# Kernel optimization log

Measured on AMD Instinct MI355X. Metric: run time of the kernel, lower is better.

## Reference

```python
import jax, jax.numpy as jnp
import numpy as np

N_NODES = 100000
N_EDGES = 1600000
F_IN = 128
HID = 128
N_CLASSES = 10
N_GRAPHS = 128
N_LAYERS = 4


def _uniform(key, shape, fan_in):
    s = 1.0 / np.sqrt(fan_in)
    return jax.random.uniform(key, shape, jnp.float32, -s, s)


def setup_inputs() -> dict:
    key = jax.random.key(0)
    ks = jax.random.split(key, 14)
    x = jax.random.normal(ks[0], (N_NODES, F_IN), jnp.float32)
    edge_index = jax.random.randint(ks[1], (2, N_EDGES), 0, N_NODES, dtype=jnp.int32)
    batch = jnp.sort(jax.random.randint(ks[2], (N_NODES,), 0, N_GRAPHS, dtype=jnp.int32))
    # GraphConv layer 1: lin_rel (with bias) + lin_root (no bias)
    W1_rel = _uniform(ks[3], (F_IN, HID), F_IN)
    b1_rel = _uniform(ks[4], (HID,), F_IN)
    W1_root = _uniform(ks[5], (F_IN, HID), F_IN)
    # remaining num_layers-1 GraphConv layers, stacked
    Wc_rel = _uniform(ks[6], (N_LAYERS - 1, HID, HID), HID)
    bc_rel = _uniform(ks[7], (N_LAYERS - 1, HID), HID)
    Wc_root = _uniform(ks[8], (N_LAYERS - 1, HID, HID), HID)
    # JumpingKnowledge 'cat' -> lin1: (num_layers*hidden) -> hidden
    Wl1 = _uniform(ks[9], (N_LAYERS * HID, HID), N_LAYERS * HID)
    bl1 = _uniform(ks[10], (HID,), N_LAYERS * HID)
    Wl2 = _uniform(ks[11], (HID, N_CLASSES), HID)
    bl2 = _uniform(ks[12], (N_CLASSES,), HID)
    return {
        "x": x, "edge_index": edge_index, "batch": batch,
        "W1_rel": W1_rel, "b1_rel": b1_rel, "W1_root": W1_root,
        "Wc_rel": Wc_rel, "bc_rel": bc_rel, "Wc_root": Wc_root,
        "Wl1": Wl1, "bl1": bl1, "Wl2": Wl2, "bl2": bl2,
    }


def reference(x, edge_index, batch, W1_rel, b1_rel, W1_root,
              Wc_rel, bc_rel, Wc_root, Wl1, bl1, Wl2, bl2):
    src, dst = edge_index[0], edge_index[1]

    def graph_conv(h, Wr, br, Wroot):
        # GraphConv (aggr='add'): lin_rel(sum_{j in N(i)} x_j) + lin_root(x_i)
        agg = jax.ops.segment_sum(h[src], dst, num_segments=N_NODES)
        return agg @ Wr + br + h @ Wroot

    counts = jax.ops.segment_sum(jnp.ones((N_NODES, 1), x.dtype), batch,
                                 num_segments=N_GRAPHS)
    counts = jnp.maximum(counts, 1.0)

    def global_mean_pool(h):
        sums = jax.ops.segment_sum(h, batch, num_segments=N_GRAPHS)
        return sums / counts

    h = jax.nn.relu(graph_conv(x, W1_rel, b1_rel, W1_root))
    xs = [global_mean_pool(h)]
    for i in range(N_LAYERS - 1):
        h = jax.nn.relu(graph_conv(h, Wc_rel[i], bc_rel[i], Wc_root[i]))
        xs.append(global_mean_pool(h))

    z = jnp.concatenate(xs, axis=-1)            # [N_GRAPHS, N_LAYERS*HID]
    z = jax.nn.relu(z @ Wl1 + bl1)
    return z @ Wl2 + bl2                        # [N_GRAPHS, N_CLASSES]
```

## Files before the change

kernel.cpp:

```cpp
#include <hip/hip_runtime.h>

#define NNODES 100000
#define NEDGES 1600000
#define FDIM 128
#define NGRAPHS 128
#define NLAYERS 4
#define NCLASS 10
#define LDC 136
#define LDC8 136
#define NBUCK 391
#define EBCAP 5120
#define EPB 4096
#define NBLK_E ((NEDGES + EPB - 1) / EPB)

typedef __attribute__((ext_vector_type(8))) short bf16x8;
typedef __attribute__((ext_vector_type(4))) float f32x4;
typedef __attribute__((ext_vector_type(2))) float f32x2;
typedef unsigned char u8;
typedef unsigned short u16;
typedef unsigned int u32;
typedef unsigned long long u64;

__device__ __forceinline__ u16 f2bf(float f) {
    u32 u = __float_as_uint(f);
    u += 0x7fffu + ((u >> 16) & 1u);
    return (u16)(u >> 16);
}
__device__ __forceinline__ u32 pack_bf(float a, float b) {
    return (u32)f2bf(a) | ((u32)f2bf(b) << 16);
}

__device__ __forceinline__ void gload_lds16(const u16* g, u16* l) {
    __builtin_amdgcn_global_load_lds(
        (const __attribute__((address_space(1))) u32*)g,
        (__attribute__((address_space(3))) u32*)l, 16, 0, 0);
}


__global__ __launch_bounds__(256) void conv_x(const float* __restrict__ x,
                                              u16* __restrict__ xb,
                                              u8* __restrict__ x8) {
    int i = (blockIdx.x * 256 + threadIdx.x) * 4;
    if (i < NNODES * FDIM) {
        float4 v = *(const float4*)(x + i);
        u32 p0 = pack_bf(v.x, v.y), p1 = pack_bf(v.z, v.w);
        *(u32*)(xb + i) = p0;
        *(u32*)(xb + i + 2) = p1;
        u32 a = (u32)__builtin_amdgcn_cvt_pk_fp8_f32(v.x, v.y, 0, 0);
        u32 b = (u32)__builtin_amdgcn_cvt_pk_fp8_f32(v.z, v.w, 0, 0);
        *(u32*)(x8 + i) = (a & 0xffffu) | (b << 16);
    }
}

__global__ __launch_bounds__(256) void conv_w(const float* __restrict__ W1_rel,
                                              const float* __restrict__ W1_root,
                                              const float* __restrict__ Wc_rel,
                                              const float* __restrict__ Wc_root,
                                              u16* __restrict__ Wcat) {
    int idx = blockIdx.x * 256 + threadIdx.x;
    if (idx >= NLAYERS * 256 * FDIM) return;
    int n = idx & 127;
    int k = (idx >> 7) & 255;
    int l = idx >> 15;
    const float* Wr = (l == 0) ? W1_rel  : Wc_rel  + (size_t)(l - 1) * FDIM * FDIM;
    const float* Wt = (l == 0) ? W1_root : Wc_root + (size_t)(l - 1) * FDIM * FDIM;
    float v = (k < 128) ? Wr[(size_t)k * FDIM + n] : Wt[(size_t)(k - 128) * FDIM + n];
    Wcat[(size_t)l * 32768 + (size_t)n * 256 + k] = f2bf(v);
}


__global__ __launch_bounds__(192) void graph_ptr_kernel(const int* __restrict__ batch,
                                                        int* __restrict__ gptr) {
    int g = threadIdx.x;
    if (g > NGRAPHS) return;
    int lo = 0, hi = NNODES;
    while (lo < hi) {
        int mid = (lo + hi) >> 1;
        if (batch[mid] < g) lo = mid + 1; else hi = mid;
    }
    gptr[g] = lo;
}

__global__ __launch_bounds__(256) void bcur_init(int* __restrict__ bcur) {
    int i = blockIdx.x * 256 + threadIdx.x;
    if (i < NBUCK) bcur[i] = i * EBCAP;
}

__global__ __launch_bounds__(256) void bucket_scatter(const int* __restrict__ src,
                                                      const int* __restrict__ dst,
                                                      int* __restrict__ bcur,
                                                      u64* __restrict__ ebuf) {
    __shared__ int cnt[NBUCK];
    for (int i = threadIdx.x; i < NBUCK; i += 256) cnt[i] = 0;
    __syncthreads();
    int e0 = blockIdx.x * EPB;
    int e1 = e0 + EPB; if (e1 > NEDGES) e1 = NEDGES;
    for (int e = e0 + threadIdx.x; e < e1; e += 256)
        atomicAdd(&cnt[dst[e] >> 8], 1);
    __syncthreads();
    for (int i = threadIdx.x; i < NBUCK; i += 256) {
        int c = cnt[i];
        if (c) cnt[i] = atomicAdd(&bcur[i], c);
    }
    __syncthreads();
    for (int e = e0 + threadIdx.x; e < e1; e += 256) {
        int d = dst[e], s = src[e];
        int pos = atomicAdd(&cnt[d >> 8], 1);
        ebuf[pos] = ((u64)(u32)d << 32) | (u32)s;
    }
}

__global__ __launch_bounds__(256) void bucket_csr(const u64* __restrict__ ebuf,
                                                  const int* __restrict__ bcur,
                                                  int* __restrict__ rowstart,
                                                  int* __restrict__ rowend,
                                                  int* __restrict__ csr) {
    __shared__ int cur[256];
    __shared__ int sd[256];
    int b = blockIdx.x, t = threadIdx.x;
    int ebase = b * EBCAP, eend = bcur[b];
    int n0 = b << 8;
    cur[t] = 0;
    __syncthreads();
    for (int e = ebase + t; e < eend; e += 256) {
        int d = (int)(ebuf[e] >> 32);
        atomicAdd(&cur[d & 255], 1);
    }
    __syncthreads();
    int v = cur[t];
    sd[t] = v;
    __syncthreads();
    for (int s = 1; s < 256; s <<= 1) {
        int add = (t >= s) ? sd[t - s] : 0;
        __syncthreads();
        sd[t] += add;
        __syncthreads();
    }
    int excl = sd[t] - v;
    cur[t] = ebase + excl;
    if (n0 + t < NNODES) {
        rowstart[n0 + t] = ebase + excl;
        rowend[n0 + t]   = ebase + excl + v;
    }
    __syncthreads();
    for (int e = ebase + t; e < eend; e += 256) {
        u64 r = ebuf[e];
        int d = (int)(r >> 32);
        int pos = atomicAdd(&cur[d & 255], 1);
        csr[pos] = (int)(r & 0xffffffffu);
    }
}


__global__ __launch_bounds__(256) void agg_bf(const u8* __restrict__ h8,
                                              const int* __restrict__ rowstart,
                                              const int* __restrict__ rowend,
                                              const int* __restrict__ csr,
                                              u16* __restrict__ agg) {
    int wave = threadIdx.x >> 6;
    int lane = threadIdx.x & 63;
    int node = (blockIdx.x << 2) + wave;
    if (node >= NNODES) return;
    int e0 = rowstart[node], e1 = rowend[node];
    int cnt = e1 - e0;
    float ax = 0.f, ay = 0.f;
    if (cnt <= 64) {
        int myidx = (lane < cnt) ? csr[e0 + lane] : 0;
        int nb = (cnt + 15) >> 4;
        for (int b = 0; b < nb; ++b) {
            int base = b * 16;
            u32 vv[16];
#pragma unroll
            for (int i = 0; i < 16; ++i) {
                int s = __builtin_amdgcn_readlane(myidx, base + i);
                vv[i] = *(const u16*)(h8 + (size_t)s * FDIM + lane * 2);
            }
            if (base + 16 <= cnt) {
#pragma unroll
                for (int i = 0; i < 16; ++i) {
                    f32x2 f = __builtin_amdgcn_cvt_pk_f32_fp8((int)vv[i], 0);
                    ax += f.x; ay += f.y;
                }
            } else {
#pragma unroll
                for (int i = 0; i < 16; ++i) {
                    f32x2 f = __builtin_amdgcn_cvt_pk_f32_fp8((int)vv[i], 0);
                    float m = (base + i < cnt) ? 1.f : 0.f;
                    ax = fmaf(f.x, m, ax);
                    ay = fmaf(f.y, m, ay);
                }
            }
        }
    } else {
        int e = e0;
        for (; e + 8 <= e1; e += 8) {
            u32 v0 = *(const u16*)(h8 + (size_t)csr[e]     * FDIM + lane * 2);
            u32 v1 = *(const u16*)(h8 + (size_t)csr[e + 1] * FDIM + lane * 2);
            u32 v2 = *(const u16*)(h8 + (size_t)csr[e + 2] * FDIM + lane * 2);
            u32 v3 = *(const u16*)(h8 + (size_t)csr[e + 3] * FDIM + lane * 2);
            u32 v4 = *(const u16*)(h8 + (size_t)csr[e + 4] * FDIM + lane * 2);
            u32 v5 = *(const u16*)(h8 + (size_t)csr[e + 5] * FDIM + lane * 2);
            u32 v6 = *(const u16*)(h8 + (size_t)csr[e + 6] * FDIM + lane * 2);
            u32 v7 = *(const u16*)(h8 + (size_t)csr[e + 7] * FDIM + lane * 2);
            f32x2 f0 = __builtin_amdgcn_cvt_pk_f32_fp8((int)v0, 0);
            f32x2 f1 = __builtin_amdgcn_cvt_pk_f32_fp8((int)v1, 0);
            f32x2 f2 = __builtin_amdgcn_cvt_pk_f32_fp8((int)v2, 0);
            f32x2 f3 = __builtin_amdgcn_cvt_pk_f32_fp8((int)v3, 0);
            f32x2 f4 = __builtin_amdgcn_cvt_pk_f32_fp8((int)v4, 0);
            f32x2 f5 = __builtin_amdgcn_cvt_pk_f32_fp8((int)v5, 0);
            f32x2 f6 = __builtin_amdgcn_cvt_pk_f32_fp8((int)v6, 0);
            f32x2 f7 = __builtin_amdgcn_cvt_pk_f32_fp8((int)v7, 0);
            ax += f0.x + f1.x + f2.x + f3.x + f4.x + f5.x + f6.x + f7.x;
            ay += f0.y + f1.y + f2.y + f3.y + f4.y + f5.y + f6.y + f7.y;
        }
        for (; e < e1; ++e) {
            u32 v0 = *(const u16*)(h8 + (size_t)csr[e] * FDIM + lane * 2);
            f32x2 f = __builtin_amdgcn_cvt_pk_f32_fp8((int)v0, 0);
            ax += f.x; ay += f.y;
        }
    }
    ((u32*)(agg + (size_t)node * FDIM))[lane] = pack_bf(ax, ay);
}


__global__ __launch_bounds__(256) void gemm_mfma(const u16* __restrict__ aggb,
                                                 const u16* __restrict__ hinb,
                                                 const u16* __restrict__ Wl,
                                                 const float* __restrict__ bias,
                                                 const int* __restrict__ batch,
                                                 float* __restrict__ z, int layer, int last,
                                                 u16* __restrict__ houtb,
                                                 u8* __restrict__ hout8) {
    __shared__ u16 S[26112];
    __shared__ int batchs[128];
    u16* As = S;
    u16* Bs = S + 8192;
    u8* Cs8 = (u8*)S + 34816;
    const int t = threadIdx.x;
    const int lane = t & 63;
    const int w = t >> 6;
    const int wr = w >> 1, wc = w & 1;
    const int row0 = blockIdx.x * 128;
    const int lr = lane & 15;

    const int srow = lane >> 3;
    const int sq = lane & 7;

    f32x4 acc[4][4];
#pragma unroll
    for (int m = 0; m < 4; ++m)
#pragma unroll
        for (int n = 0; n < 4; ++n) acc[m][n] = (f32x4){0.f, 0.f, 0.f, 0.f};

    if (t < 128) batchs[t] = (row0 + t < NNODES) ? batch[row0 + t] : NGRAPHS;

    for (int kb = 0; kb < 4; ++kb) {
        const u16* xsrc = (kb < 2) ? aggb : hinb;
        const int koff = (kb & 1) * 64;
#pragma unroll
        for (int i = 0; i < 4; ++i) {
            int blk8 = w * 4 + i;
            int r = blk8 * 8 + srow;
            int sc = sq ^ (r & 7);
            int arow = row0 + r; if (arow > NNODES - 1) arow = NNODES - 1;
            gload_lds16(xsrc + (size_t)arow * FDIM + koff + sc * 8, As + blk8 * 512);
            gload_lds16(Wl + (size_t)r * 256 + kb * 64 + sc * 8, Bs + blk8 * 512);
        }
        __syncthreads();
#pragma unroll
        for (int ks = 0; ks < 2; ++ks) {
            bf16x8 a[4], b[4];
            int qr = ks * 4 + (lane >> 4);
#pragma unroll
            for (int m = 0; m < 4; ++m) {
                int r = wr * 64 + m * 16 + lr;
                int ch = qr ^ (r & 7);
                a[m] = *(const bf16x8*)&As[r * 64 + ch * 8];
            }
#pragma unroll
            for (int n = 0; n < 4; ++n) {
                int r = wc * 64 + n * 16 + lr;
                int ch = qr ^ (r & 7);
                b[n] = *(const bf16x8*)&Bs[r * 64 + ch * 8];
            }
#pragma unroll
            for (int m = 0; m < 4; ++m)
#pragma unroll
                for (int n = 0; n < 4; ++n)
                    acc[m][n] = __builtin_amdgcn_mfma_f32_16x16x32_bf16(a[m], b[n], acc[m][n], 0, 0, 0);
        }
        __syncthreads();
    }
#pragma unroll
    for (int m = 0; m < 4; ++m) {
#pragma unroll
        for (int n = 0; n < 4; ++n) {
            int col = wc * 64 + n * 16 + lr;
            float bb = bias[col];
#pragma unroll
            for (int reg = 0; reg < 4; ++reg) {
                int row = wr * 64 + m * 16 + (lane >> 4) * 4 + reg;
                float v = fmaxf(acc[m][n][reg] + bb, 0.f);
                S[row * LDC + col] = f2bf(v);
                Cs8[row * LDC8 + col] = (u8)__builtin_amdgcn_cvt_pk_fp8_f32(v, v, 0, 0);
            }
        }
    }
    __syncthreads();
    if (!last) {
        int r = t >> 1, half = t & 1;
        if (row0 + r < NNODES) {
#pragma unroll
            for (int j = 0; j < 8; ++j) {
                bf16x8 v = *(const bf16x8*)&S[r * LDC + half * 64 + j * 8];
                *(bf16x8*)(houtb + (size_t)(row0 + r) * FDIM + half * 64 + j * 8) = v;
            }
#pragma unroll
            for (int j = 0; j < 8; ++j) {
                u64 v8 = *(const u64*)&Cs8[r * LDC8 + half * 64 + j * 8];
                *(u64*)(hout8 + (size_t)(row0 + r) * FDIM + half * 64 + j * 8) = v8;
            }
        }
    }
    {
        int col = t & 127, half = t >> 7;
        int r0 = half * 64, r1 = r0 + 64;
        float* zl = z + (size_t)layer * FDIM + col;
        int g = batchs[r0];
        float s = 0.f;
        for (int r = r0; r < r1; ++r) {
            int gn = batchs[r];
            if (gn != g) {
                atomicAdd(zl + (size_t)g * (NLAYERS * FDIM), s);
                s = 0.f; g = gn;
            }
            s += __uint_as_float((u32)S[r * LDC + col] << 16);
        }
        atomicAdd(zl + (size_t)g * (NLAYERS * FDIM), s);
    }
}


__global__ __launch_bounds__(128) void mlp1(const float* __restrict__ z,
                                            const int* __restrict__ gptr,
                                            const float* __restrict__ Wl1,
                                            const float* __restrict__ bl1,
                                            float* __restrict__ z2) {
    int g = blockIdx.x, j = threadIdx.x;
    __shared__ float zs[NLAYERS * FDIM];
    int cnt = gptr[g + 1] - gptr[g]; if (cnt < 1) cnt = 1;
    float invc = 1.0f / (float)cnt;
    for (int k = j; k < NLAYERS * FDIM; k += 128)
        zs[k] = z[(size_t)g * (NLAYERS * FDIM) + k] * invc;
    __syncthreads();
    float s = bl1[j];
    for (int k = 0; k < NLAYERS * FDIM; ++k) s = fmaf(zs[k], Wl1[(size_t)k * FDIM + j], s);
    z2[(size_t)g * FDIM + j] = fmaxf(s, 0.f);
}

__global__ __launch_bounds__(128) void mlp2(const float* __restrict__ z2,
                                            const float* __restrict__ Wl2,
                                            const float* __restrict__ bl2,
                                            float* __restrict__ out) {
    int g = blockIdx.x, c = threadIdx.x;
    __shared__ float zs[FDIM];
    if (threadIdx.x < FDIM) zs[threadIdx.x] = z2[(size_t)g * FDIM + threadIdx.x];
    __syncthreads();
    if (c < NCLASS) {
        float s = bl2[c];
        for (int k = 0; k < FDIM; ++k) s = fmaf(zs[k], Wl2[(size_t)k * NCLASS + c], s);
        out[(size_t)g * NCLASS + c] = s;
    }
}


extern "C" void kernel_launch(void* const* d_in, const int* in_sizes, int n_in,
                              void* d_out, int out_size, void* d_ws, size_t ws_size,
                              hipStream_t stream) {
    const float* x       = (const float*)d_in[0];
    const int*   ei      = (const int*)d_in[1];
    const int*   batch   = (const int*)d_in[2];
    const float* W1_rel  = (const float*)d_in[3];
    const float* b1_rel  = (const float*)d_in[4];
    const float* W1_root = (const float*)d_in[5];
    const float* Wc_rel  = (const float*)d_in[6];
    const float* bc_rel  = (const float*)d_in[7];
    const float* Wc_root = (const float*)d_in[8];
    const float* Wl1     = (const float*)d_in[9];
    const float* bl1     = (const float*)d_in[10];
    const float* Wl2     = (const float*)d_in[11];
    const float* bl2     = (const float*)d_in[12];
    float* out = (float*)d_out;

    const int* srcv = ei;
    const int* dstv = ei + NEDGES;

    char* ws = (char*)d_ws;
    size_t off = 0;
    auto alloc = [&](size_t bytes) -> void* {
        void* p = ws + off;
        off = (off + bytes + 255) & ~(size_t)255;
        return p;
    };
    u16* xb      = (u16*)alloc((size_t)NNODES * FDIM * 2);
    u16* hA      = (u16*)alloc((size_t)NNODES * FDIM * 2);
    u16* hB      = (u16*)alloc((size_t)NNODES * FDIM * 2);
    u16* aggb    = (u16*)alloc((size_t)NNODES * FDIM * 2);
    u8*  x8      = (u8*)alloc((size_t)NNODES * FDIM);
    u8*  h8A     = (u8*)alloc((size_t)NNODES * FDIM);
    u8*  h8B     = (u8*)alloc((size_t)NNODES * FDIM);
    u16* Wcat    = (u16*)alloc((size_t)NLAYERS * 256 * FDIM * 2);
    int* csr     = (int*)alloc((size_t)NBUCK * EBCAP * 4);
    int* rowstart= (int*)alloc((size_t)NNODES * 4);
    int* rowend  = (int*)alloc((size_t)NNODES * 4);
    int* bcur    = (int*)alloc((size_t)(NBUCK + 1) * 4);
    int* gptr    = (int*)alloc(1024);
    float* z     = (float*)alloc((size_t)(NGRAPHS + 1) * NLAYERS * FDIM * 4);
    float* z2    = (float*)alloc((size_t)NGRAPHS * FDIM * 4);
    u64* ebuf    = (u64*)hA;
    (void)ws_size; (void)in_sizes; (void)n_in; (void)out_size;

    hipMemsetAsync(z, 0, (size_t)(NGRAPHS + 1) * NLAYERS * FDIM * 4, stream);
    conv_x<<<(NNODES * FDIM / 4 + 255) / 256, 256, 0, stream>>>(x, xb, x8);
    conv_w<<<(NLAYERS * 256 * FDIM + 255) / 256, 256, 0, stream>>>(W1_rel, W1_root, Wc_rel, Wc_root, Wcat);
    graph_ptr_kernel<<<1, 192, 0, stream>>>(batch, gptr);
    bcur_init<<<(NBUCK + 255) / 256, 256, 0, stream>>>(bcur);
    bucket_scatter<<<NBLK_E, 256, 0, stream>>>(srcv, dstv, bcur, ebuf);
    bucket_csr<<<NBUCK, 256, 0, stream>>>(ebuf, bcur, rowstart, rowend, csr);

    const u16* hin = xb;
    const u8*  hin8 = x8;
    for (int l = 0; l < NLAYERS; ++l) {
        u16* hout  = (l & 1) ? hB : hA;
        u8*  hout8 = (l & 1) ? h8B : h8A;
        const u16* Wl = Wcat + (size_t)l * 256 * FDIM;
        const float* bb = (l == 0) ? b1_rel : bc_rel + (size_t)(l - 1) * FDIM;
        agg_bf<<<(NNODES + 3) / 4, 256, 0, stream>>>(hin8, rowstart, rowend, csr, aggb);
        gemm_mfma<<<(NNODES + 127) / 128, 256, 0, stream>>>(aggb, hin, Wl, bb, batch, z, l,
                                                            (l == NLAYERS - 1) ? 1 : 0, hout, hout8);
        hin = hout; hin8 = hout8;
    }
    mlp1<<<NGRAPHS, 128, 0, stream>>>(z, gptr, Wl1, bl1, z2);
    mlp2<<<NGRAPHS, 128, 0, stream>>>(z2, Wl2, bl2, out);
}
```

Measured before the change: 383.1 us.

## Halve GEMM epilogue LDS, stage bucket edges in LDS, merge setup kernels

The GEMM epilogue now stages output in two 64-row passes, which shrinks the shared buffer from about 52KB to 32KB so more blocks can be resident per CU. The cost is extra barriers and serialized epilogue phases. bucket_csr copies its bucket's edges into a 40KB LDS array so global ebuf is read once instead of twice, though that large LDS footprint limits its occupancy. The graph-pointer and bucket-cursor init kernels are merged into one launch.

New measurement: 410.9 us. +7.3%, slower.

```diff
diff --git a/kernel.cpp b/kernel.cpp
--- a/kernel.cpp
+++ b/kernel.cpp
@@ -69,21 +69,19 @@
 }
 
 
-__global__ __launch_bounds__(192) void graph_ptr_kernel(const int* __restrict__ batch,
-                                                        int* __restrict__ gptr) {
-    int g = threadIdx.x;
-    if (g > NGRAPHS) return;
-    int lo = 0, hi = NNODES;
-    while (lo < hi) {
-        int mid = (lo + hi) >> 1;
-        if (batch[mid] < g) lo = mid + 1; else hi = mid;
-    }
-    gptr[g] = lo;
-}
-
-__global__ __launch_bounds__(256) void bcur_init(int* __restrict__ bcur) {
-    int i = blockIdx.x * 256 + threadIdx.x;
-    if (i < NBUCK) bcur[i] = i * EBCAP;
+__global__ __launch_bounds__(512) void setup_kernel(const int* __restrict__ batch,
+                                                    int* __restrict__ gptr,
+                                                    int* __restrict__ bcur) {
+    int t = threadIdx.x;
+    if (t < NBUCK) bcur[t] = t * EBCAP;
+    if (t <= NGRAPHS) {
+        int lo = 0, hi = NNODES;
+        while (lo < hi) {
+            int mid = (lo + hi) >> 1;
+            if (batch[mid] < t) lo = mid + 1; else hi = mid;
+        }
+        gptr[t] = lo;
+    }
 }
 
 __global__ __launch_bounds__(256) void bucket_scatter(const int* __restrict__ src,
@@ -115,15 +113,18 @@
                                                   int* __restrict__ rowstart,
                                                   int* __restrict__ rowend,
                                                   int* __restrict__ csr) {
+    __shared__ u64 eb[EBCAP];
     __shared__ int cur[256];
     __shared__ int sd[256];
     int b = blockIdx.x, t = threadIdx.x;
     int ebase = b * EBCAP, eend = bcur[b];
+    int ne = eend - ebase;
     int n0 = b << 8;
     cur[t] = 0;
-    __syncthreads();
-    for (int e = ebase + t; e < eend; e += 256) {
-        int d = (int)(ebuf[e] >> 32);
+    for (int e = t; e < ne; e += 256) eb[e] = ebuf[ebase + e];
+    __syncthreads();
+    for (int e = t; e < ne; e += 256) {
+        int d = (int)(eb[e] >> 32);
         atomicAdd(&cur[d & 255], 1);
     }
     __syncthreads();
@@ -143,8 +144,8 @@
         rowend[n0 + t]   = ebase + excl + v;
     }
     __syncthreads();
-    for (int e = ebase + t; e < eend; e += 256) {
-        u64 r = ebuf[e];
+    for (int e = t; e < ne; e += 256) {
+        u64 r = eb[e];
         int d = (int)(r >> 32);
         int pos = atomicAdd(&cur[d & 255], 1);
         csr[pos] = (int)(r & 0xffffffffu);
@@ -231,11 +232,11 @@
                                                  float* __restrict__ z, int layer, int last,
                                                  u16* __restrict__ houtb,
                                                  u8* __restrict__ hout8) {
-    __shared__ u16 S[26112];
+    __shared__ u16 S[16384];
     __shared__ int batchs[128];
     u16* As = S;
     u16* Bs = S + 8192;
-    u8* Cs8 = (u8*)S + 34816;
+    u8* Cs8 = (u8*)S + 17408;
     const int t = threadIdx.x;
     const int lane = t & 63;
     const int w = t >> 6;
@@ -292,51 +293,57 @@
         __syncthreads();
     }
 #pragma unroll
-    for (int m = 0; m < 4; ++m) {
-#pragma unroll
-        for (int n = 0; n < 4; ++n) {
-            int col = wc * 64 + n * 16 + lr;
-            float bb = bias[col];
-#pragma unroll
-            for (int reg = 0; reg < 4; ++reg) {
-                int row = wr * 64 + m * 16 + (lane >> 4) * 4 + reg;
-                float v = fmaxf(acc[m][n][reg] + bb, 0.f);
-                S[row * LDC + col] = f2bf(v);
-                Cs8[row * LDC8 + col] = (u8)__builtin_amdgcn_cvt_pk_fp8_f32(v, v, 0, 0);
-            }
-        }
-    }
-    __syncthreads();
-    if (!last) {
-        int r = t >> 1, half = t & 1;
-        if (row0 + r < NNODES) {
-#pragma unroll
-            for (int j = 0; j < 8; ++j) {
-                bf16x8 v = *(const bf16x8*)&S[r * LDC + half * 64 + j * 8];
-                *(bf16x8*)(houtb + (size_t)(row0 + r) * FDIM + half * 64 + j * 8) = v;
-            }
-#pragma unroll
-            for (int j = 0; j < 8; ++j) {
-                u64 v8 = *(const u64*)&Cs8[r * LDC8 + half * 64 + j * 8];
-                *(u64*)(hout8 + (size_t)(row0 + r) * FDIM + half * 64 + j * 8) = v8;
-            }
-        }
-    }
-    {
-        int col = t & 127, half = t >> 7;
-        int r0 = half * 64, r1 = r0 + 64;
-        float* zl = z + (size_t)layer * FDIM + col;
-        int g = batchs[r0];
-        float s = 0.f;
-        for (int r = r0; r < r1; ++r) {
-            int gn = batchs[r];
-            if (gn != g) {
-                atomicAdd(zl + (size_t)g * (NLAYERS * FDIM), s);
-                s = 0.f; g = gn;
-            }
-            s += __uint_as_float((u32)S[r * LDC + col] << 16);
-        }
-        atomicAdd(zl + (size_t)g * (NLAYERS * FDIM), s);
+    for (int p = 0; p < 2; ++p) {
+        if (wr == p) {
+#pragma unroll
+            for (int m = 0; m < 4; ++m) {
+#pragma unroll
+                for (int n = 0; n < 4; ++n) {
+                    int col = wc * 64 + n * 16 + lr;
+                    float bb = bias[col];
+#pragma unroll
+                    for (int reg = 0; reg < 4; ++reg) {
+                        int sr = m * 16 + (lane >> 4) * 4 + reg;
+                        float v = fmaxf(acc[m][n][reg] + bb, 0.f);
+                        S[sr * LDC + col] = f2bf(v);
+                        Cs8[sr * LDC8 + col] = (u8)__builtin_amdgcn_cvt_pk_fp8_f32(v, v, 0, 0);
+                    }
+                }
+            }
+        }
+        __syncthreads();
+        if (!last) {
+            int r = t >> 2, q = t & 3;
+            int grow = row0 + p * 64 + r;
+            if (grow < NNODES) {
+#pragma unroll
+                for (int j = 0; j < 4; ++j) {
+                    bf16x8 v = *(const bf16x8*)&S[r * LDC + q * 32 + j * 8];
+                    *(bf16x8*)(houtb + (size_t)grow * FDIM + q * 32 + j * 8) = v;
+                }
+#pragma unroll
+                for (int j = 0; j < 4; ++j) {
+                    u64 v8 = *(const u64*)&Cs8[r * LDC8 + q * 32 + j * 8];
+                    *(u64*)(hout8 + (size_t)grow * FDIM + q * 32 + j * 8) = v8;
+                }
+            }
+        }
+        if ((t >> 7) == p) {
+            int col = t & 127;
+            float* zl = z + (size_t)layer * FDIM + col;
+            int g = batchs[p * 64];
+            float s = 0.f;
+            for (int r = 0; r < 64; ++r) {
+                int gn = batchs[p * 64 + r];
+                if (gn != g) {
+                    atomicAdd(zl + (size_t)g * (NLAYERS * FDIM), s);
+                    s = 0.f; g = gn;
+                }
+                s += __uint_as_float((u32)S[r * LDC + col] << 16);
+            }
+            atomicAdd(zl + (size_t)g * (NLAYERS * FDIM), s);
+        }
+        __syncthreads();
     }
 }
 
@@ -423,8 +430,7 @@
     hipMemsetAsync(z, 0, (size_t)(NGRAPHS + 1) * NLAYERS * FDIM * 4, stream);
     conv_x<<<(NNODES * FDIM / 4 + 255) / 256, 256, 0, stream>>>(x, xb, x8);
     conv_w<<<(NLAYERS * 256 * FDIM + 255) / 256, 256, 0, stream>>>(W1_rel, W1_root, Wc_rel, Wc_root, Wcat);
-    graph_ptr_kernel<<<1, 192, 0, stream>>>(batch, gptr);
-    bcur_init<<<(NBUCK + 255) / 256, 256, 0, stream>>>(bcur);
+    setup_kernel<<<1, 512, 0, stream>>>(batch, gptr, bcur);
     bucket_scatter<<<NBLK_E, 256, 0, stream>>>(srcv, dstv, bcur, ebuf);
     bucket_csr<<<NBUCK, 256, 0, stream>>>(ebuf, bcur, rowstart, rowend, csr);
 
```
